# Kernel tuning notes

Hardware: AMD Instinct MI355X
Metric: run time of the kernel (lower is better)

## Reference

```python
import jax, jax.numpy as jnp
import numpy as np

CUTOFF = 5.0
EPS = 1e-3  # keras BatchNormalization default epsilon
L = 3       # num_interactions
N = 100000
E = 1600000
H = 64
FIN = 16


def setup_inputs() -> dict:
    key = jax.random.key(0)
    ks = jax.random.split(key, 16)
    s = 0.1  # weight scale for numerical stability
    return {
        "x": jax.random.normal(ks[0], (N, FIN), jnp.float32),
        "edge_index": jax.random.randint(ks[1], (2, E), 0, N, jnp.int32),
        "distances": jax.random.uniform(ks[2], (E,), jnp.float32) * CUTOFF,
        "edge_attr": jax.random.normal(ks[3], (E, 1), jnp.float32),
        "emb_W": jax.random.normal(ks[4], (FIN, H), jnp.float32) * s,
        "emb_b": jnp.zeros((H,), jnp.float32),
        "fW1": jax.random.normal(ks[5], (L, 1, H), jnp.float32) * s,
        "fb1": jnp.zeros((L, H), jnp.float32),
        "fW2": jax.random.normal(ks[6], (L, H, H), jnp.float32) * s,
        "fb2": jnp.zeros((L, H), jnp.float32),
        "iW1": jax.random.normal(ks[7], (L, H, H), jnp.float32) * s,
        "ib1": jnp.zeros((L, H), jnp.float32),
        "iW2": jax.random.normal(ks[8], (L, H, H), jnp.float32) * s,
        "ib2": jnp.zeros((L, H), jnp.float32),
        "bn_gamma": jnp.ones((L, H), jnp.float32),
        "bn_beta": jnp.zeros((L, H), jnp.float32),
        "oW1": jax.random.normal(ks[9], (H, H // 2), jnp.float32) * s,
        "ob1": jnp.zeros((H // 2,), jnp.float32),
        "og1": jnp.ones((H // 2,), jnp.float32),
        "obt1": jnp.zeros((H // 2,), jnp.float32),
        "oW2": jax.random.normal(ks[10], (H // 2, H // 2), jnp.float32) * s,
        "ob2": jnp.zeros((H // 2,), jnp.float32),
        "og2": jnp.ones((H // 2,), jnp.float32),
        "obt2": jnp.zeros((H // 2,), jnp.float32),
        "fin_W": jax.random.normal(ks[11], (H // 2, 3), jnp.float32) * s,
        "fin_b": jnp.zeros((3,), jnp.float32),
    }


def reference(x, edge_index, distances, edge_attr,
              emb_W, emb_b, fW1, fb1, fW2, fb2,
              iW1, ib1, iW2, ib2, bn_gamma, bn_beta,
              oW1, ob1, og1, obt1, oW2, ob2, og2, obt2,
              fin_W, fin_b):
    n_nodes = x.shape[0]
    row, col = edge_index[0], edge_index[1]
    inv = 1.0 / jnp.sqrt(1.0 + EPS)  # BN inference with moving mean=0, var=1

    # shared edge-level quantities
    scaled = distances * (2.0 / CUTOFF) - 1.0                       # [E]
    cut = 0.5 * (jnp.cos(distances * np.pi / CUTOFF) + 1.0)
    cut = jnp.where(distances <= CUTOFF, cut, 0.0)                  # [E]

    h = x @ emb_W + emb_b                                           # [N,H]
    for l in range(L):
        # filter MLP: [E,1] -> [E,F]
        f = jnp.tanh(scaled[:, None] * fW1[l][0] + fb1[l]) @ fW2[l] + fb2[l]
        f = f * cut[:, None]
        # original: sum_F(neighbor[:,None,:] * f[:,:,None]) == neighbor * sum_F(f)
        fs = f.sum(-1)                                              # [E]
        msgs = h[col] * fs[:, None]                                 # [E,H] gather
        agg = jax.ops.segment_sum(msgs, row, num_segments=n_nodes)  # [N,H] scatter-add
        out = jax.nn.softplus(agg @ iW1[l] + ib1[l]) @ iW2[l] + ib2[l]
        out = out * inv * bn_gamma[l] + bn_beta[l]                  # BN (inference)
        h = h + out

    g = h.mean(axis=0)                                              # [H]
    g = jax.nn.softplus(g @ oW1 + ob1) * inv * og1 + obt1
    g = jax.nn.softplus(g @ oW2 + ob2) * inv * og2 + obt2
    return g @ fin_W + fin_b                                        # [3]
```

## Files before the change

kernel.cpp:

```cpp
#include <hip/hip_runtime.h>
#include <hip/hip_fp16.h>
#include <math.h>

#define CUTOFF 5.0f
#define H 64
#define FIN 16
#define NLAYERS 3
#define LUTN 2048
#define LUTSTRIDE 2052
#define ASTRIDE 72
#define MEANB 256
#define BROWS 256
#define NBMAX 512
#define MAXC 5120
#define ABLK 4096
#define NREP 4

#define BN_INV 0.999500374750f

typedef _Float16 h8 __attribute__((ext_vector_type(8)));
typedef _Float16 h2 __attribute__((ext_vector_type(2)));
typedef float f32x4 __attribute__((ext_vector_type(4)));
typedef unsigned int u32x2 __attribute__((ext_vector_type(2)));

__device__ __forceinline__ float softplus_f(float x) {
    return fmaxf(x, 0.f) + __logf(1.f + __expf(-fabsf(x)));
}

__global__ __launch_bounds__(1024)
void k_pre(const float* __restrict__ x, const float* __restrict__ emb_W,
           const float* __restrict__ emb_b, _Float16* __restrict__ h0,
           const float* __restrict__ fW1, const float* __restrict__ fb1,
           const float* __restrict__ fW2, const float* __restrict__ fb2,
           const float* __restrict__ iW1, const float* __restrict__ iW2,
           const float* __restrict__ bn_g, const float* __restrict__ bn_b,
           const float* __restrict__ ib2, h8* __restrict__ Wsw,
           float* __restrict__ b2p, float* __restrict__ lut,
           const int* __restrict__ ei, const float* __restrict__ dist,
           unsigned int* __restrict__ cursor, u32x2* __restrict__ stg,
           int N, int E, int NB, int nbA, int nbE16) {
    __shared__ u32x2 s_rec[ABLK];
    __shared__ unsigned s_cnt[NBMAX * NREP];
    __shared__ unsigned s_tot[NBMAX];
    __shared__ unsigned s_gst[NBMAX * NREP];
    __shared__ unsigned s_gbase[NBMAX];
    __shared__ float swsum[64];
    __shared__ float sbsum;
    int b = blockIdx.x;
    int t = threadIdx.x;
    if (b < nbA) {
        int e0 = b * ABLK;
        int nE = min(ABLK, E - e0);
        int gg = t >> 8;
        for (int i = t; i < NBMAX * NREP; i += 1024) s_cnt[i] = 0;
        __syncthreads();
        int rowv[4];
        unsigned rxv[4] = {0u, 0u, 0u, 0u};
        unsigned rkv[4] = {0u, 0u, 0u, 0u};
#pragma unroll
        for (int j = 0; j < 4; j++) {
            int li = j * 1024 + t;
            rowv[j] = -1;
            if (li < nE) {
                int e = e0 + li;
                int r = ei[e];
                int col = ei[E + e];
                float d = dist[e];
                int didx = (int)(d * (32768.0f / CUTOFF) + 0.5f);
                didx = max(0, min(didx, 32767));
                rowv[j] = r;
                rxv[j] = ((unsigned)col << 15) | (unsigned)didx;
                rkv[j] = atomicAdd(&s_cnt[(r / BROWS) * NREP + gg], 1u);
            }
        }
        __syncthreads();
        unsigned tot = 0;
        if (t < NBMAX) {
            tot = s_cnt[t * NREP] + s_cnt[t * NREP + 1] +
                  s_cnt[t * NREP + 2] + s_cnt[t * NREP + 3];
            s_tot[t] = tot;
        }
        __syncthreads();
        for (int off = 1; off < NBMAX; off <<= 1) {
            unsigned v = 0;
            if (t < NBMAX && t >= off) v = s_tot[t - off];
            __syncthreads();
            if (t < NBMAX) s_tot[t] += v;
            __syncthreads();
        }
        if (t < NBMAX) {
            unsigned lstart = s_tot[t] - tot;
            unsigned runb = lstart;
#pragma unroll
            for (int g = 0; g < NREP; g++) {
                s_gst[t * NREP + g] = runb;
                runb += s_cnt[t * NREP + g];
            }
            s_tot[t] = lstart;
            s_gbase[t] = (tot && t < (unsigned)NB) ? atomicAdd(&cursor[t], tot) : 0u;
        }
        __syncthreads();
#pragma unroll
        for (int j = 0; j < 4; j++) {
            if (rowv[j] >= 0) {
                int bk = rowv[j] / BROWS;
                unsigned slot = s_gst[bk * NREP + gg] + rkv[j];
                u32x2 rec;
                rec.x = rxv[j];
                rec.y = (unsigned)rowv[j];
                s_rec[slot] = rec;
            }
        }
        __syncthreads();
        for (int i = t; i < nE; i += 1024) {
            u32x2 rec = s_rec[i];
            int bk = (int)(rec.y / BROWS);
            unsigned g = s_gbase[bk] + ((unsigned)i - s_tot[bk]);
            if (g < MAXC)
                stg[(size_t)bk * MAXC + g] = rec;
        }
    } else if (b < nbA + nbE16) {
        int lane = t & 63;
        int w = t >> 6;
        int node = (b - nbA) * 16 + w;
        if (node < N) {
            float acc = emb_b[lane];
#pragma unroll
            for (int k = 0; k < FIN; k++) acc += x[node * FIN + k] * emb_W[k * H + lane];
            h0[(size_t)node * H + lane] = (_Float16)acc;
        }
    } else if (b < nbA + nbE16 + NLAYERS * 3) {
        int lb = b - nbA - nbE16;
        int l = lb / 3, part = lb % 3;
        if (t < 64) {
            float s = 0.f;
            for (int j = 0; j < H; j++) s += fW2[l * H * H + t * H + j];
            swsum[t] = s;
        }
        if (t == 64) {
            float s = 0.f;
            for (int j = 0; j < H; j++) s += fb2[l * H + j];
            sbsum = s;
        }
        __syncthreads();
        int i = part * 1024 + t;
        if (i <= LUTN) {
            float d = (float)i * (CUTOFF / (float)LUTN);
            float scaled = d * (2.0f / CUTOFF) - 1.0f;
            float cut = 0.5f * (__cosf(d * (3.14159265358979f / CUTOFF)) + 1.0f);
            if (d > CUTOFF) cut = 0.f;
            float s = 0.f;
            for (int hh = 0; hh < H; hh++) {
                int wi = l * H + hh;
                s += tanhf(scaled * fW1[wi] + fb1[wi]) * swsum[hh];
            }
            lut[l * LUTSTRIDE + i] = cut * (s + sbsum);
        }
    } else {
        int tid = (b - nbA - nbE16 - NLAYERS * 3) * 1024 + t;
        if (tid < NLAYERS * H)
            b2p[tid] = ib2[tid] * BN_INV * bn_g[tid] + bn_b[tid];
        if (tid < NLAYERS * 2 * 8 * 64) {
            int lane = tid & 63;
            int frag = (tid >> 6) & 7;
            int mat  = (tid >> 9) & 1;
            int l    = tid >> 10;
            int kt = frag >> 2, nt = frag & 3;
            int n = nt * 16 + (lane & 15);
            int k0 = kt * 32 + (lane >> 4) * 8;
            const float* W = (mat ? iW2 : iW1) + l * H * H;
            float scale = mat ? BN_INV * bn_g[l * H + n] : 1.0f;
            h8 v;
#pragma unroll
            for (int j = 0; j < 8; j++) v[j] = (_Float16)(W[(k0 + j) * H + n] * scale);
            Wsw[tid] = v;
        }
    }
}

__global__ __launch_bounds__(1024)
void k_passB(const u32x2* __restrict__ stg, const unsigned int* __restrict__ cursor,
             int* __restrict__ row_ptr, unsigned int* __restrict__ recs,
             int N, int NB) {
    __shared__ int s_bb[NBMAX];
    __shared__ unsigned s_c[BROWS * NREP];
    __shared__ unsigned s_t[BROWS];
    __shared__ unsigned s_g[BROWS * NREP];
    __shared__ unsigned s_out[MAXC];
    int b = blockIdx.x, t = threadIdx.x;
    int gg = t >> 8;
    if (t < NBMAX) {
        int cb = 0;
        if (t < NB) cb = min((int)cursor[t], MAXC);
        s_bb[t] = cb;
    }
    __syncthreads();
    for (int off = 1; off < NBMAX; off <<= 1) {
        int v = 0;
        if (t < NBMAX && t >= off) v = s_bb[t - off];
        __syncthreads();
        if (t < NBMAX) s_bb[t] += v;
        __syncthreads();
    }
    int bbase = (b > 0) ? s_bb[b - 1] : 0;
    int cnt = s_bb[b] - bbase;
    int r0 = b * BROWS;
    int r1 = min(r0 + BROWS, N);
    int nrows = r1 - r0;
    const u32x2* mystg = stg + (size_t)b * MAXC;
    for (int i = t; i < BROWS * NREP; i += 1024) s_c[i] = 0;
    __syncthreads();
    u32x2 myrec[5];
    unsigned myrk[5] = {0u, 0u, 0u, 0u, 0u};
    int nm = 0;
#pragma unroll
    for (int i = 0; i < 5; i++) {
        int idx = t + i * 1024;
        if (idx < cnt) {
            myrec[i] = mystg[idx];
            myrk[i] = atomicAdd(&s_c[((int)myrec[i].y - r0) * NREP + gg], 1u);
            nm = i + 1;
        }
    }
    __syncthreads();
    unsigned tot = 0;
    if (t < BROWS) {
        tot = s_c[t * NREP] + s_c[t * NREP + 1] +
              s_c[t * NREP + 2] + s_c[t * NREP + 3];
        s_t[t] = tot;
    }
    __syncthreads();
    for (int off = 1; off < BROWS; off <<= 1) {
        unsigned v = 0;
        if (t < BROWS && t >= off) v = s_t[t - off];
        __syncthreads();
        if (t < BROWS) s_t[t] += v;
        __syncthreads();
    }
    if (t < BROWS) {
        unsigned excl = s_t[t] - tot;
        if (t < nrows) row_ptr[r0 + t] = bbase + (int)excl;
        unsigned runb = excl;
#pragma unroll
        for (int g = 0; g < NREP; g++) {
            s_g[t * NREP + g] = runb;
            runb += s_c[t * NREP + g];
        }
    }
    if (b == NB - 1 && t == 0) row_ptr[N] = bbase + cnt;
    __syncthreads();
#pragma unroll
    for (int i = 0; i < 5; i++)
        if (i < nm) {
            unsigned slot = s_g[((int)myrec[i].y - r0) * NREP + gg] + myrk[i];
            s_out[slot] = myrec[i].x;
        }
    __syncthreads();
    for (int i = t; i < cnt; i += 1024)
        recs[bbase + i] = s_out[i];
}

#define PROC4(KK, SS, TT, ACC) do {                                          \
    int _lim = ((TT) > (SS)) ? (TT) - 1 : 0;                                 \
    int _ka = min((KK), _lim),     _kb = min((KK) + 1, _lim);                \
    int _kc = min((KK) + 2, _lim), _kd = min((KK) + 3, _lim);                \
    unsigned _ra = recs[_ka], _rb = recs[_kb];                               \
    unsigned _rc = recs[_kc], _rd = recs[_kd];                               \
    float _ta = (float)(_ra & 32767u) * (1.0f / 16.0f);                      \
    float _tb = (float)(_rb & 32767u) * (1.0f / 16.0f);                      \
    float _tc = (float)(_rc & 32767u) * (1.0f / 16.0f);                      \
    float _td = (float)(_rd & 32767u) * (1.0f / 16.0f);                      \
    int _ia = (int)_ta, _ib = (int)_tb, _ic = (int)_tc, _id = (int)_td;      \
    float _fa = s_lut[_ia], _fb = s_lut[_ib];                                \
    float _fc = s_lut[_ic], _fd = s_lut[_id];                                \
    float _va = _fa + (_ta - (float)_ia) * (s_lut[_ia + 1] - _fa);           \
    float _vb = _fb + (_tb - (float)_ib) * (s_lut[_ib + 1] - _fb);           \
    float _vc = _fc + (_tc - (float)_ic) * (s_lut[_ic + 1] - _fc);           \
    float _vd = _fd + (_td - (float)_id) * (s_lut[_id + 1] - _fd);           \
    _va = ((KK)     < (TT)) ? _va : 0.f;                                     \
    _vb = ((KK) + 1 < (TT)) ? _vb : 0.f;                                     \
    _vc = ((KK) + 2 < (TT)) ? _vc : 0.f;                                     \
    _vd = ((KK) + 3 < (TT)) ? _vd : 0.f;                                     \
    union { uint4 u; h2 v[4]; } _pa, _pb, _pc, _pd;                          \
    _pa.u = h4[(_ra >> 15) * 8u + (unsigned)ci];                             \
    _pb.u = h4[(_rb >> 15) * 8u + (unsigned)ci];                             \
    _pc.u = h4[(_rc >> 15) * 8u + (unsigned)ci];                             \
    _pd.u = h4[(_rd >> 15) * 8u + (unsigned)ci];                             \
    _Float16 _ha = (_Float16)_va, _hb = (_Float16)_vb;                       \
    _Float16 _hc = (_Float16)_vc, _hd = (_Float16)_vd;                       \
    h2 _aa = (h2){_ha, _ha}, _ab = (h2){_hb, _hb};                           \
    h2 _ac = (h2){_hc, _hc}, _ad = (h2){_hd, _hd};                           \
    _Pragma("unroll")                                                        \
    for (int _q = 0; _q < 4; _q++) (ACC)[_q] += _aa * _pa.v[_q];             \
    _Pragma("unroll")                                                        \
    for (int _q = 0; _q < 4; _q++) (ACC)[_q] += _ab * _pb.v[_q];             \
    _Pragma("unroll")                                                        \
    for (int _q = 0; _q < 4; _q++) (ACC)[_q] += _ac * _pc.v[_q];             \
    _Pragma("unroll")                                                        \
    for (int _q = 0; _q < 4; _q++) (ACC)[_q] += _ad * _pd.v[_q];             \
} while (0)

__global__ __launch_bounds__(256, 6)
void k_layer(const int* __restrict__ row_ptr, const unsigned int* __restrict__ recs,
             const float* __restrict__ lutl, const h8* __restrict__ Wsw,
             const float* __restrict__ b1, const float* __restrict__ b2p,
             const _Float16* __restrict__ h_in, _Float16* __restrict__ h_out,
             float* __restrict__ pA, int N, int last) {
    __shared__ float s_lut[LUTN + 1];
    __shared__ _Float16 sA[64 * ASTRIDE];
    for (int i = threadIdx.x; i <= LUTN; i += 256) s_lut[i] = lutl[i];
    __syncthreads();

    int lane = threadIdx.x & 63;
    int w = threadIdx.x >> 6;
    int base = blockIdx.x * 64 + w * 16;
    int g = lane >> 3, ci = lane & 7;
    const uint4* h4 = (const uint4*)h_in;

    {
        int node0 = base + g;
        int node1 = base + 8 + g;
        h2 acc0[4], acc1[4];
#pragma unroll
        for (int q = 0; q < 4; q++) {
            acc0[q] = (h2){(_Float16)0.f, (_Float16)0.f};
            acc1[q] = (h2){(_Float16)0.f, (_Float16)0.f};
        }
        int s0 = 0, t0 = 0, s1 = 0, t1 = 0;
        if (node0 < N) { s0 = row_ptr[node0]; t0 = row_ptr[node0 + 1]; }
        if (node1 < N) { s1 = row_ptr[node1]; t1 = row_ptr[node1 + 1]; }
        int it0 = (t0 - s0 + 3) >> 2;
        int it1 = (t1 - s1 + 3) >> 2;
        int iters = max(it0, it1);
        for (int it = 0; it < iters; ++it) {
            int k0 = s0 + it * 4;
            int k1 = s1 + it * 4;
            PROC4(k0, s0, t0, acc0);
            PROC4(k1, s1, t1, acc1);
        }
        union { uint4 u4; h2 v[4]; } pk;
#pragma unroll
        for (int q = 0; q < 4; q++) pk.v[q] = acc0[q];
        *(uint4*)&sA[(size_t)(w * 16 + g) * ASTRIDE + ci * 8] = pk.u4;
#pragma unroll
        for (int q = 0; q < 4; q++) pk.v[q] = acc1[q];
        *(uint4*)&sA[(size_t)(w * 16 + 8 + g) * ASTRIDE + ci * 8] = pk.u4;
    }

    int q4 = lane >> 4, c16 = lane & 15;
    int rowb = w * 16;
    const h8* WB1 = Wsw;
    const h8* WB2 = Wsw + 8 * 64;
    h8 A0 = *(const h8*)&sA[(size_t)(rowb + c16) * ASTRIDE + q4 * 8];
    h8 A1 = *(const h8*)&sA[(size_t)(rowb + c16) * ASTRIDE + 32 + q4 * 8];
    f32x4 C1[4];
#pragma unroll
    for (int nt = 0; nt < 4; nt++) {
        f32x4 c = {0.f, 0.f, 0.f, 0.f};
        c = __builtin_amdgcn_mfma_f32_16x16x32_f16(A0, WB1[nt * 64 + lane], c, 0, 0, 0);
        c = __builtin_amdgcn_mfma_f32_16x16x32_f16(A1, WB1[(4 + nt) * 64 + lane], c, 0, 0, 0);
        C1[nt] = c;
    }
#pragma unroll
    for (int nt = 0; nt < 4; nt++) {
        float bb = b1[nt * 16 + c16];
#pragma unroll
        for (int reg = 0; reg < 4; reg++) {
            float v = softplus_f(C1[nt][reg] + bb);
            sA[(size_t)(rowb + q4 * 4 + reg) * ASTRIDE + nt * 16 + c16] = (_Float16)v;
        }
    }
    h8 M0 = *(const h8*)&sA[(size_t)(rowb + c16) * ASTRIDE + q4 * 8];
    h8 M1 = *(const h8*)&sA[(size_t)(rowb + c16) * ASTRIDE + 32 + q4 * 8];
    f32x4 C2[4];
#pragma unroll
    for (int nt = 0; nt < 4; nt++) {
        f32x4 c = {0.f, 0.f, 0.f, 0.f};
        c = __builtin_amdgcn_mfma_f32_16x16x32_f16(M0, WB2[nt * 64 + lane], c, 0, 0, 0);
        c = __builtin_amdgcn_mfma_f32_16x16x32_f16(M1, WB2[(4 + nt) * 64 + lane], c, 0, 0, 0);
        C2[nt] = c;
    }
    if (!last) {
#pragma unroll
        for (int nt = 0; nt < 4; nt++) {
            float bb2 = b2p[nt * 16 + c16];
#pragma unroll
            for (int reg = 0; reg < 4; reg++) {
                int node = base + q4 * 4 + reg;
                if (node < N) {
                    size_t idx = (size_t)node * H + nt * 16 + c16;
                    float hn = (float)h_in[idx] + C2[nt][reg] + bb2;
                    h_out[idx] = (_Float16)hn;
                }
            }
        }
    } else {
        float ps[4];
#pragma unroll
        for (int nt = 0; nt < 4; nt++) {
            float bb2 = b2p[nt * 16 + c16];
            float s = 0.f;
#pragma unroll
            for (int reg = 0; reg < 4; reg++) {
                int node = base + q4 * 4 + reg;
                if (node < N) {
                    size_t idx = (size_t)node * H + nt * 16 + c16;
                    s += (float)h_in[idx] + C2[nt][reg] + bb2;
                }
            }
            ps[nt] = s;
        }
#pragma unroll
        for (int nt = 0; nt < 4; nt++) {
            float v = ps[nt];
            v += __shfl_xor(v, 16, 64);
            v += __shfl_xor(v, 32, 64);
            if (lane < 16)
                pA[((size_t)blockIdx.x * 4 + w) * H + nt * 16 + c16] = v;
        }
    }
}

__global__ __launch_bounds__(256)
void k_mean(const float* __restrict__ pA, float* __restrict__ partials, int P) {
    __shared__ float s_r[4][H];
    int lane = threadIdx.x & 63;
    int w = threadIdx.x >> 6;
    int wg = blockIdx.x * 4 + w;
    int stride = gridDim.x * 4;
    float local = 0.f;
    for (int i = wg; i < P; i += stride) local += pA[(size_t)i * H + lane];
    s_r[w][lane] = local;
    __syncthreads();
    if (w == 0) {
        float s = s_r[0][lane] + s_r[1][lane] + s_r[2][lane] + s_r[3][lane];
        partials[(size_t)blockIdx.x * H + lane] = s;
    }
}

__global__ __launch_bounds__(256)
void k_final(const float* __restrict__ partials, int N,
             const float* __restrict__ oW1, const float* __restrict__ ob1,
             const float* __restrict__ og1, const float* __restrict__ obt1,
             const float* __restrict__ oW2, const float* __restrict__ ob2,
             const float* __restrict__ og2, const float* __restrict__ obt2,
             const float* __restrict__ fin_W, const float* __restrict__ fin_b,
             float* __restrict__ out) {
    __shared__ float red[4][H];
    __shared__ float sg[H], su[H / 2], sv[H / 2];
    int t = threadIdx.x;
    int ch = t & 63, grp = t >> 6;
    float s = 0.f;
    for (int b = grp; b < MEANB; b += 4) s += partials[(size_t)b * H + ch];
    red[grp][ch] = s;
    __syncthreads();
    if (t < H) sg[t] = (red[0][t] + red[1][t] + red[2][t] + red[3][t]) / (float)N;
    __syncthreads();
    int j = t;
    if (j < H / 2) {
        float acc = ob1[j];
        for (int k = 0; k < H; k++) acc += sg[k] * oW1[k * (H / 2) + j];
        su[j] = softplus_f(acc) * BN_INV * og1[j] + obt1[j];
    }
    __syncthreads();
    if (j < H / 2) {
        float acc = ob2[j];
        for (int k = 0; k < H / 2; k++) acc += su[k] * oW2[k * (H / 2) + j];
        sv[j] = softplus_f(acc) * BN_INV * og2[j] + obt2[j];
    }
    __syncthreads();
    if (j < 3) {
        float acc = fin_b[j];
        for (int k = 0; k < H / 2; k++) acc += sv[k] * fin_W[k * 3 + j];
        out[j] = acc;
    }
}

extern "C" void kernel_launch(void* const* d_in, const int* in_sizes, int n_in,
                              void* d_out, int out_size, void* d_ws, size_t ws_size,
                              hipStream_t stream) {
    const float* x      = (const float*)d_in[0];
    const int*   ei     = (const int*)d_in[1];
    const float* dist   = (const float*)d_in[2];
    const float* emb_W  = (const float*)d_in[4];
    const float* emb_b  = (const float*)d_in[5];
    const float* fW1    = (const float*)d_in[6];
    const float* fb1    = (const float*)d_in[7];
    const float* fW2    = (const float*)d_in[8];
    const float* fb2    = (const float*)d_in[9];
    const float* iW1    = (const float*)d_in[10];
    const float* ib1    = (const float*)d_in[11];
    const float* iW2    = (const float*)d_in[12];
    const float* ib2    = (const float*)d_in[13];
    const float* bn_g   = (const float*)d_in[14];
    const float* bn_b   = (const float*)d_in[15];
    const float* oW1    = (const float*)d_in[16];
    const float* ob1    = (const float*)d_in[17];
    const float* og1    = (const float*)d_in[18];
    const float* obt1   = (const float*)d_in[19];
    const float* oW2    = (const float*)d_in[20];
    const float* ob2    = (const float*)d_in[21];
    const float* og2    = (const float*)d_in[22];
    const float* obt2   = (const float*)d_in[23];
    const float* fin_W  = (const float*)d_in[24];
    const float* fin_b  = (const float*)d_in[25];
    float* out = (float*)d_out;

    int N = in_sizes[0] / FIN;
    int E = in_sizes[2];
    int NB = (N + BROWS - 1) / BROWS;
    int nb_tile = (N + 63) / 64;
    int P = nb_tile * 4;

    float*  ws   = (float*)d_ws;
    _Float16* h0 = (_Float16*)ws;
    _Float16* h1 = h0 + (size_t)N * H;
    unsigned int* recs = (unsigned int*)(h1 + (size_t)N * H);
    h8*     Wsw  = (h8*)(recs + E);
    float*  lut  = (float*)(Wsw + NLAYERS * 2 * 8 * 64);
    float*  partials = lut + 3 * LUTSTRIDE;
    float*  b2p  = partials + MEANB * H;
    float*  pA   = b2p + NLAYERS * H;
    u32x2*  stg  = (u32x2*)(pA + (size_t)P * H);
    int*    row_ptr = (int*)(stg + (size_t)NBMAX * MAXC);
    unsigned int* cursor = (unsigned int*)(row_ptr + N + 1);

    hipMemsetAsync(cursor, 0, NBMAX * sizeof(unsigned int), stream);

    int nbA = (E + ABLK - 1) / ABLK;
    int nbE16 = (N + 15) / 16;
    int nb_pre = nbA + nbE16 + NLAYERS * 3 + 3;
    k_pre<<<nb_pre, 1024, 0, stream>>>(x, emb_W, emb_b, h0,
                                       fW1, fb1, fW2, fb2, iW1, iW2,
                                       bn_g, bn_b, ib2, Wsw, b2p, lut,
                                       ei, dist, cursor, stg,
                                       N, E, NB, nbA, nbE16);

    k_passB<<<NB, 1024, 0, stream>>>(stg, cursor, row_ptr, recs, N, NB);

    _Float16* hp[2] = {h0, h1};
    for (int l = 0; l < NLAYERS; l++) {
        k_layer<<<nb_tile, 256, 0, stream>>>(row_ptr, recs, lut + (size_t)l * LUTSTRIDE,
                                             Wsw + (size_t)l * 1024,
                                             ib1 + l * H, b2p + l * H,
                                             hp[l & 1], hp[(l + 1) & 1], pA, N,
                                             (l == NLAYERS - 1) ? 1 : 0);
    }

    k_mean<<<MEANB, 256, 0, stream>>>(pA, partials, P);
    k_final<<<1, 256, 0, stream>>>(partials, N, oW1, ob1, og1, obt1,
                                   oW2, ob2, og2, obt2, fin_W, fin_b, out);
}
```

Before: 323.5 us.

## Transpose shared bucket counters and compute embedding one node per thread

Shared-memory bucket counters in the edge-binning and pass-B kernels switch from bucket-major to replica-major layout. Atomics from different thread groups on the same bucket then land in separate banks. The embedding branch now gives each node to one thread: it loads the 16 inputs as float4 from x, reads the weights staged in shared memory, and writes 8-half vectors. This replaces 64 lanes per node reading x and emb_W from global, at the cost of more registers and far fewer embedding blocks.

```diff
diff --git a/kernel.cpp b/kernel.cpp
--- a/kernel.cpp
+++ b/kernel.cpp
@@ -38,12 +38,14 @@
            float* __restrict__ b2p, float* __restrict__ lut,
            const int* __restrict__ ei, const float* __restrict__ dist,
            unsigned int* __restrict__ cursor, u32x2* __restrict__ stg,
-           int N, int E, int NB, int nbA, int nbE16) {
+           int N, int E, int NB, int nbA, int nbE) {
     __shared__ u32x2 s_rec[ABLK];
-    __shared__ unsigned s_cnt[NBMAX * NREP];
+    __shared__ unsigned s_cnt[NREP * NBMAX];
     __shared__ unsigned s_tot[NBMAX];
-    __shared__ unsigned s_gst[NBMAX * NREP];
+    __shared__ unsigned s_gst[NREP * NBMAX];
     __shared__ unsigned s_gbase[NBMAX];
+    __shared__ float sW[FIN * H];
+    __shared__ float sB[H];
     __shared__ float swsum[64];
     __shared__ float sbsum;
     int b = blockIdx.x;
@@ -52,7 +54,7 @@
         int e0 = b * ABLK;
         int nE = min(ABLK, E - e0);
         int gg = t >> 8;
-        for (int i = t; i < NBMAX * NREP; i += 1024) s_cnt[i] = 0;
+        for (int i = t; i < NREP * NBMAX; i += 1024) s_cnt[i] = 0;
         __syncthreads();
         int rowv[4];
         unsigned rxv[4] = {0u, 0u, 0u, 0u};
@@ -70,14 +72,14 @@
                 didx = max(0, min(didx, 32767));
                 rowv[j] = r;
                 rxv[j] = ((unsigned)col << 15) | (unsigned)didx;
-                rkv[j] = atomicAdd(&s_cnt[(r / BROWS) * NREP + gg], 1u);
+                rkv[j] = atomicAdd(&s_cnt[gg * NBMAX + r / BROWS], 1u);
             }
         }
         __syncthreads();
         unsigned tot = 0;
         if (t < NBMAX) {
-            tot = s_cnt[t * NREP] + s_cnt[t * NREP + 1] +
-                  s_cnt[t * NREP + 2] + s_cnt[t * NREP + 3];
+            tot = s_cnt[t] + s_cnt[NBMAX + t] +
+                  s_cnt[2 * NBMAX + t] + s_cnt[3 * NBMAX + t];
             s_tot[t] = tot;
         }
         __syncthreads();
@@ -93,8 +95,8 @@
             unsigned runb = lstart;
 #pragma unroll
             for (int g = 0; g < NREP; g++) {
-                s_gst[t * NREP + g] = runb;
-                runb += s_cnt[t * NREP + g];
+                s_gst[g * NBMAX + t] = runb;
+                runb += s_cnt[g * NBMAX + t];
             }
             s_tot[t] = lstart;
             s_gbase[t] = (tot && t < (unsigned)NB) ? atomicAdd(&cursor[t], tot) : 0u;
@@ -104,7 +106,7 @@
         for (int j = 0; j < 4; j++) {
             if (rowv[j] >= 0) {
                 int bk = rowv[j] / BROWS;
-                unsigned slot = s_gst[bk * NREP + gg] + rkv[j];
+                unsigned slot = s_gst[gg * NBMAX + bk] + rkv[j];
                 u32x2 rec;
                 rec.x = rxv[j];
                 rec.y = (unsigned)rowv[j];
@@ -119,18 +121,40 @@
             if (g < MAXC)
                 stg[(size_t)bk * MAXC + g] = rec;
         }
-    } else if (b < nbA + nbE16) {
-        int lane = t & 63;
-        int w = t >> 6;
-        int node = (b - nbA) * 16 + w;
+    } else if (b < nbA + nbE) {
+        if (t < FIN * H) sW[t] = emb_W[t];
+        if (t < H) sB[t] = emb_b[t];
+        __syncthreads();
+        int node = (b - nbA) * 1024 + t;
         if (node < N) {
-            float acc = emb_b[lane];
-#pragma unroll
-            for (int k = 0; k < FIN; k++) acc += x[node * FIN + k] * emb_W[k * H + lane];
-            h0[(size_t)node * H + lane] = (_Float16)acc;
-        }
-    } else if (b < nbA + nbE16 + NLAYERS * 3) {
-        int lb = b - nbA - nbE16;
+            const float4* x4 = (const float4*)(x) + (size_t)node * (FIN / 4);
+            float4 q0 = x4[0], q1 = x4[1], q2 = x4[2], q3 = x4[3];
+            float xr[FIN] = {q0.x, q0.y, q0.z, q0.w, q1.x, q1.y, q1.z, q1.w,
+                             q2.x, q2.y, q2.z, q2.w, q3.x, q3.y, q3.z, q3.w};
+            _Float16* hp = h0 + (size_t)node * H;
+#pragma unroll
+            for (int half = 0; half < 2; half++) {
+                float acc[32];
+#pragma unroll
+                for (int c = 0; c < 32; c++) acc[c] = sB[half * 32 + c];
+#pragma unroll
+                for (int k = 0; k < FIN; k++) {
+                    float xv = xr[k];
+#pragma unroll
+                    for (int c = 0; c < 32; c++)
+                        acc[c] += xv * sW[k * H + half * 32 + c];
+                }
+#pragma unroll
+                for (int c8 = 0; c8 < 4; c8++) {
+                    h8 v;
+#pragma unroll
+                    for (int j = 0; j < 8; j++) v[j] = (_Float16)acc[c8 * 8 + j];
+                    *(h8*)(hp + half * 32 + c8 * 8) = v;
+                }
+            }
+        }
+    } else if (b < nbA + nbE + NLAYERS * 3) {
+        int lb = b - nbA - nbE;
         int l = lb / 3, part = lb % 3;
         if (t < 64) {
             float s = 0.f;
@@ -157,7 +181,7 @@
             lut[l * LUTSTRIDE + i] = cut * (s + sbsum);
         }
     } else {
-        int tid = (b - nbA - nbE16 - NLAYERS * 3) * 1024 + t;
+        int tid = (b - nbA - nbE - NLAYERS * 3) * 1024 + t;
         if (tid < NLAYERS * H)
             b2p[tid] = ib2[tid] * BN_INV * bn_g[tid] + bn_b[tid];
         if (tid < NLAYERS * 2 * 8 * 64) {
@@ -183,9 +207,9 @@
              int* __restrict__ row_ptr, unsigned int* __restrict__ recs,
              int N, int NB) {
     __shared__ int s_bb[NBMAX];
-    __shared__ unsigned s_c[BROWS * NREP];
+    __shared__ unsigned s_c[NREP * BROWS];
     __shared__ unsigned s_t[BROWS];
-    __shared__ unsigned s_g[BROWS * NREP];
+    __shared__ unsigned s_g[NREP * BROWS];
     __shared__ unsigned s_out[MAXC];
     int b = blockIdx.x, t = threadIdx.x;
     int gg = t >> 8;
@@ -208,7 +232,7 @@
     int r1 = min(r0 + BROWS, N);
     int nrows = r1 - r0;
     const u32x2* mystg = stg + (size_t)b * MAXC;
-    for (int i = t; i < BROWS * NREP; i += 1024) s_c[i] = 0;
+    for (int i = t; i < NREP * BROWS; i += 1024) s_c[i] = 0;
     __syncthreads();
     u32x2 myrec[5];
     unsigned myrk[5] = {0u, 0u, 0u, 0u, 0u};
@@ -218,15 +242,14 @@
         int idx = t + i * 1024;
         if (idx < cnt) {
             myrec[i] = mystg[idx];
-            myrk[i] = atomicAdd(&s_c[((int)myrec[i].y - r0) * NREP + gg], 1u);
+            myrk[i] = atomicAdd(&s_c[gg * BROWS + ((int)myrec[i].y - r0)], 1u);
             nm = i + 1;
         }
     }
     __syncthreads();
     unsigned tot = 0;
     if (t < BROWS) {
-        tot = s_c[t * NREP] + s_c[t * NREP + 1] +
-              s_c[t * NREP + 2] + s_c[t * NREP + 3];
+        tot = s_c[t] + s_c[BROWS + t] + s_c[2 * BROWS + t] + s_c[3 * BROWS + t];
         s_t[t] = tot;
     }
     __syncthreads();
@@ -243,8 +266,8 @@
         unsigned runb = excl;
 #pragma unroll
         for (int g = 0; g < NREP; g++) {
-            s_g[t * NREP + g] = runb;
-            runb += s_c[t * NREP + g];
+            s_g[g * BROWS + t] = runb;
+            runb += s_c[g * BROWS + t];
         }
     }
     if (b == NB - 1 && t == 0) row_ptr[N] = bbase + cnt;
@@ -252,7 +275,7 @@
 #pragma unroll
     for (int i = 0; i < 5; i++)
         if (i < nm) {
-            unsigned slot = s_g[((int)myrec[i].y - r0) * NREP + gg] + myrk[i];
+            unsigned slot = s_g[gg * BROWS + ((int)myrec[i].y - r0)] + myrk[i];
             s_out[slot] = myrec[i].x;
         }
     __syncthreads();
@@ -528,13 +551,13 @@
     hipMemsetAsync(cursor, 0, NBMAX * sizeof(unsigned int), stream);
 
     int nbA = (E + ABLK - 1) / ABLK;
-    int nbE16 = (N + 15) / 16;
-    int nb_pre = nbA + nbE16 + NLAYERS * 3 + 3;
+    int nbE = (N + 1023) / 1024;
+    int nb_pre = nbA + nbE + NLAYERS * 3 + 3;
     k_pre<<<nb_pre, 1024, 0, stream>>>(x, emb_W, emb_b, h0,
                                        fW1, fb1, fW2, fb2, iW1, iW2,
                                        bn_g, bn_b, ib2, Wsw, b2p, lut,
                                        ei, dist, cursor, stg,
-                                       N, E, NB, nbA, nbE16);
+                                       N, E, NB, nbA, nbE);
 
     k_passB<<<NB, 1024, 0, stream>>>(stg, cursor, row_ptr, recs, N, NB);
 
```

After: 299.5 us. 1.08x faster.
